# Kernel tuning notes

Measured on AMD Instinct MI355X. Metric: run time of the kernel, lower is better.

Reference implementation:

```python
import jax, jax.numpy as jnp
import numpy as np

KERNEL = 3            # MONAI default kernel_size
SMOOTH_NR = 0.0       # MONAI default
SMOOTH_DR = 1e-5      # MONAI default


def _box_sum_3d(x, k=KERNEL):
    """Separable 3D box-filter sum with zero padding ('same' output), over the
    three trailing spatial axes of a [B, C, X, Y, Z] tensor. Uses cumsum
    differences (one pass per axis) instead of 5 dense conv launches."""
    p = k // 2
    for ax in (2, 3, 4):
        pads = [(0, 0)] * x.ndim
        pads[ax] = (p + 1, p)  # extra leading zero so window sum = c[i+k]-c[i]
        c = jnp.cumsum(jnp.pad(x, pads), axis=ax)
        n = c.shape[ax]
        x = jax.lax.slice_in_dim(c, k, n, axis=ax) - jax.lax.slice_in_dim(c, 0, n - k, axis=ax)
    return x


def setup_inputs() -> dict:
    key = jax.random.key(0)
    k1, k2 = jax.random.split(key)
    shape = (2, 1, 192, 192, 192)
    pred = jax.random.uniform(k1, shape, dtype=jnp.float32)
    label = jax.random.uniform(k2, shape, dtype=jnp.float32)
    return {"pred": pred, "label": label}


def reference(pred, label):
    # Faithful to monai.losses.LocalNormalizedCrossCorrelationLoss defaults
    # (spatial_dims=3, rectangular kernel_size=3, reduction='mean').
    kernel_vol = jnp.asarray(float(KERNEL ** 3), dtype=pred.dtype)  # 27
    t, p = label, pred

    t_sum = _box_sum_3d(t)
    p_sum = _box_sum_3d(p)
    t2_sum = _box_sum_3d(t * t)
    p2_sum = _box_sum_3d(p * p)
    tp_sum = _box_sum_3d(t * p)

    t_avg = t_sum / kernel_vol
    p_avg = p_sum / kernel_vol

    cross = tp_sum - p_avg * t_sum                      # local cross-covariance * vol
    t_var = jnp.maximum(t2_sum - t_avg * t_sum, 0.0)    # local var * vol, clamped
    p_var = jnp.maximum(p2_sum - p_avg * p_sum, 0.0)

    ncc = (cross * cross + SMOOTH_NR) / (t_var * p_var + SMOOTH_DR)
    return -jnp.mean(ncc)
```

## Files before the change

### kernel.cpp

```cpp
#include <hip/hip_runtime.h>

typedef float v2f __attribute__((ext_vector_type(2)));

constexpr int NX = 192, NY = 192, NZ = 192, NB = 2;
constexpr int ZPT  = 4;
constexpr int TZ   = NZ / ZPT;
constexpr int BY   = 4;
constexpr int XSEG = 4;
constexpr int BLOCK_THREADS = TZ * BY;
constexpr int PLANE = NY * NZ;
constexpr int NXB = NX / XSEG;
constexpr int NYB = NY / BY;
constexpr int NBLK = NYB * NXB * NB;
constexpr int RSTR = 196;
constexpr int TILE_F = 2 * 6 * RSTR;

template<bool SAFE>
__device__ __forceinline__ void foldLDS(const float* __restrict__ buf,
    int ty, int z0, const float wy[3], int dm, int de, float wzm, float wze,
    float wx, v2f W[5][2])
{
    v2f S[5][3];
    #pragma unroll
    for (int r = 0; r < 3; ++r) {
        const float* Lt = buf + (ty + r) * RSTR;
        const float* Lp = Lt + 6 * RSTR;
        const float4 t4 = *reinterpret_cast<const float4*>(Lt + z0);
        const float4 p4 = *reinterpret_cast<const float4*>(Lp + z0);
        const float tm = Lt[z0 - dm] * wzm, te = Lt[z0 + de] * wze;
        const float pm = Lp[z0 - dm] * wzm, pe = Lp[z0 + de] * wze;
        v2f T[3]  = { v2f{tm, t4.x}, v2f{t4.y, t4.z}, v2f{t4.w, te} };
        v2f Pv[3] = { v2f{pm, p4.x}, v2f{p4.y, p4.z}, v2f{p4.w, pe} };
        if (!SAFE) {
            const float wr = wx * wy[r];
            #pragma unroll
            for (int q = 0; q < 3; ++q) { T[q] *= wr; Pv[q] *= wr; }
        }
        #pragma unroll
        for (int q = 0; q < 3; ++q) {
            if (r == 0) {
                S[0][q] = T[q];  S[1][q] = Pv[q];
                S[2][q] = T[q] * T[q];  S[3][q] = Pv[q] * Pv[q];  S[4][q] = T[q] * Pv[q];
            } else {
                S[0][q] += T[q];  S[1][q] += Pv[q];
                S[2][q] += T[q] * T[q];  S[3][q] += Pv[q] * Pv[q];  S[4][q] += T[q] * Pv[q];
            }
        }
    }
    #pragma unroll
    for (int q = 0; q < 5; ++q) {
        const float s0 = S[q][0].x, s1 = S[q][0].y, s2 = S[q][1].x;
        const float s3 = S[q][1].y, s4 = S[q][2].x, s5 = S[q][2].y;
        const float m12 = s1 + s2, m34 = s3 + s4;
        W[q][0] = v2f{s0 + m12, m12 + s3};
        W[q][1] = v2f{s2 + m34, m34 + s5};
    }
}

__device__ __forceinline__ float epilogue4(const v2f P[5][2], const v2f Wn[5][2])
{
    constexpr float inv_vol = 1.0f / 27.0f;
    float acc = 0.f;
    #pragma unroll
    for (int h = 0; h < 2; ++h) {
        const v2f st  = P[0][h] + Wn[0][h];
        const v2f sp  = P[1][h] + Wn[1][h];
        const v2f st2 = P[2][h] + Wn[2][h];
        const v2f sp2 = P[3][h] + Wn[3][h];
        const v2f stp = P[4][h] + Wn[4][h];
        const v2f tavg = st * inv_vol;
        const v2f pavg = sp * inv_vol;
        const v2f cross = stp - pavg * st;
        const v2f tvp   = st2 - tavg * st;
        const v2f pvp   = sp2 - pavg * sp;
        const v2f cc    = cross * cross;
        #pragma unroll
        for (int c = 0; c < 2; ++c) {
            const float tvar = fmaxf(tvp[c], 0.f);
            const float pvar = fmaxf(pvp[c], 0.f);
            acc += cc[c] * __builtin_amdgcn_rcpf(fmaf(tvar, pvar, 1e-5f));
        }
    }
    return acc;
}

template<bool SAFE>
__device__ __forceinline__ float march(
    const float* sb0, const float* sb1, const float* sb2,
    int lo0, int lo1, int lo2,
    float (*tile)[TILE_F],
    int ty, int z0, const float wy[3],
    int dm, int de, float wzm, float wze, int xs0)
{
    v2f U[5][2], V[5][2], P[5][2];
    float acc = 0.f;
    float4 G0, G1, G2;

#define XOFF(K) (SAFE ? (xs0 - 1 + (K)) * PLANE \
                      : min(max(xs0 - 1 + (K), 0), NX - 1) * PLANE)
#define WXK(K)  (SAFE ? 1.f : (((unsigned)(xs0 - 1 + (K)) < (unsigned)NX) ? 1.f : 0.f))
#define GLOAD(K) do { const int _xo = XOFF(K);                                  \
        G0 = *reinterpret_cast<const float4*>(sb0 + _xo);                       \
        G1 = *reinterpret_cast<const float4*>(sb1 + _xo);                       \
        G2 = *reinterpret_cast<const float4*>(sb2 + _xo); } while (0)
#define DSWR(K) do { float* _d = tile[(K) & 1];                                 \
        *reinterpret_cast<float4*>(_d + lo0) = G0;                              \
        *reinterpret_cast<float4*>(_d + lo1) = G1;                              \
        *reinterpret_cast<float4*>(_d + lo2) = G2; } while (0)
#define FOLD(K, WDST) foldLDS<SAFE>(tile[(K) & 1], ty, z0, wy, dm, de, wzm, wze, WXK(K), WDST)
#define PSET(A, B) do { _Pragma("unroll")                                       \
        for (int q = 0; q < 5; ++q) { _Pragma("unroll")                         \
            for (int h = 0; h < 2; ++h) P[q][h] = A[q][h] + B[q][h]; } } while (0)

    GLOAD(0); DSWR(0); __syncthreads();
    GLOAD(1); FOLD(0, U);             DSWR(1); __syncthreads();
    GLOAD(2); FOLD(1, V); PSET(U, V); DSWR(2); __syncthreads();
    GLOAD(3); FOLD(2, U); acc += epilogue4(P, U); PSET(V, U); DSWR(3); __syncthreads();
    GLOAD(4); FOLD(3, V); acc += epilogue4(P, V); PSET(U, V); DSWR(4); __syncthreads();
    GLOAD(5); FOLD(4, U); acc += epilogue4(P, U); PSET(V, U); DSWR(5); __syncthreads();
              FOLD(5, V); acc += epilogue4(P, V);

#undef XOFF
#undef WXK
#undef GLOAD
#undef DSWR
#undef FOLD
#undef PSET
    return acc;
}

__global__ __launch_bounds__(BLOCK_THREADS, 3)
void ncc_partial(const float* __restrict__ pred, const float* __restrict__ label,
                 float* __restrict__ partials)
{
    __shared__ alignas(16) float tile[2][TILE_F];

    const int tx  = threadIdx.x;
    const int ty  = threadIdx.y;
    const int tid = tx + ty * TZ;
    const int z0  = tx * ZPT;
    const int y0  = blockIdx.x * BY;
    const int y   = y0 + ty;
    const int xs0 = blockIdx.y * XSEG;
    const int b   = blockIdx.z;
    const int bbase = b * NX * PLANE;

    const float* sb[3];
    int lo[3];
    #pragma unroll
    for (int r = 0; r < 3; ++r) {
        const int j   = r * BLOCK_THREADS + tid;
        const int tt  = j / 288, rem = j - tt * 288;
        const int row = rem / 48, z4 = rem - row * 48;
        int grow = y0 - 1 + row;
        grow = min(max(grow, 0), NY - 1);
        sb[r] = (tt ? pred : label) + bbase + grow * NZ + z4 * 4;
        lo[r] = (tt * 6 + row) * RSTR + z4 * 4;
    }

    float wy[3];
    #pragma unroll
    for (int r = 0; r < 3; ++r) {
        const int yy = y + r - 1;
        wy[r] = ((unsigned)yy < (unsigned)NY) ? 1.f : 0.f;
    }
    const int   dm  = (tx == 0) ? 0 : 1;
    const int   de  = (tx == TZ - 1) ? 0 : ZPT;
    const float wzm = (tx == 0) ? 0.f : 1.f;
    const float wze = (tx == TZ - 1) ? 0.f : 1.f;

    const bool safe = (blockIdx.x >= 1) && (blockIdx.x <= NYB - 2) &&
                      (blockIdx.y >= 1) && (blockIdx.y <= NXB - 2);

    const float acc = safe
        ? march<true >(sb[0], sb[1], sb[2], lo[0], lo[1], lo[2], tile,
                       ty, z0, wy, dm, de, wzm, wze, xs0)
        : march<false>(sb[0], sb[1], sb[2], lo[0], lo[1], lo[2], tile,
                       ty, z0, wy, dm, de, wzm, wze, xs0);

    float a = acc;
    #pragma unroll
    for (int o = 32; o > 0; o >>= 1)
        a += __shfl_down(a, o, 64);

    __shared__ float wsum[BLOCK_THREADS / 64];
    if ((tid & 63) == 0) wsum[tid >> 6] = a;
    __syncthreads();
    if (tid == 0) {
        float s = 0.f;
        #pragma unroll
        for (int w = 0; w < BLOCK_THREADS / 64; ++w) s += wsum[w];
        partials[blockIdx.x + (int)gridDim.x * (blockIdx.y + (int)gridDim.y * blockIdx.z)] = s;
    }
}

__global__ __launch_bounds__(256)
void ncc_reduce(const float* __restrict__ partials, int n, float* __restrict__ out)
{
    __shared__ double sh[256];
    double s = 0.0;
    for (int i = threadIdx.x; i < n; i += 256) s += (double)partials[i];
    sh[threadIdx.x] = s;
    __syncthreads();
    for (int off = 128; off > 0; off >>= 1) {
        if ((int)threadIdx.x < off) sh[threadIdx.x] += sh[threadIdx.x + off];
        __syncthreads();
    }
    if (threadIdx.x == 0) {
        const double nvox = (double)NB * NX * NY * NZ;
        out[0] = (float)(-sh[0] / nvox);
    }
}

extern "C" void kernel_launch(void* const* d_in, const int* in_sizes, int n_in,
                              void* d_out, int out_size, void* d_ws, size_t ws_size,
                              hipStream_t stream) {
    const float* pred  = (const float*)d_in[0];
    const float* label = (const float*)d_in[1];
    float* out = (float*)d_out;
    float* partials = (float*)d_ws;

    dim3 block(TZ, BY, 1);
    dim3 grid(NYB, NXB, NB);

    ncc_partial<<<grid, block, 0, stream>>>(pred, label, partials);
    ncc_reduce<<<1, 256, 0, stream>>>(partials, NBLK, out);
}
```

Baseline: 49.60 us.

## Double x-segment per block and zero-pad LDS rows to drop z-edge masking

Each block now marches over 8 x-planes instead of 4, so the two halo planes loaded per segment are spread over more output planes and there are half as many blocks. The march is written as a rolled loop over two ping-pong LDS buffers. LDS rows gain zeroed pad cells at the z boundaries, which removes the per-thread z-edge offsets and weight multiplies in the fold. The cost is fewer blocks, which means less parallelism and a longer serial chain per block, and the halo layout becomes slightly more complex.

```diff
diff --git a/kernel.cpp b/kernel.cpp
--- a/kernel.cpp
+++ b/kernel.cpp
@@ -6,29 +6,30 @@
 constexpr int ZPT  = 4;
 constexpr int TZ   = NZ / ZPT;
 constexpr int BY   = 4;
-constexpr int XSEG = 4;
+constexpr int XSEG = 8;
 constexpr int BLOCK_THREADS = TZ * BY;
 constexpr int PLANE = NY * NZ;
 constexpr int NXB = NX / XSEG;
 constexpr int NYB = NY / BY;
 constexpr int NBLK = NYB * NXB * NB;
 constexpr int RSTR = 196;
-constexpr int TILE_F = 2 * 6 * RSTR;
+constexpr int NROWS = 12;
+constexpr int TILE_F = NROWS * RSTR + 4;
+constexpr int PADS   = (NROWS + 1) * 4;
 
 template<bool SAFE>
 __device__ __forceinline__ void foldLDS(const float* __restrict__ buf,
-    int ty, int z0, const float wy[3], int dm, int de, float wzm, float wze,
-    float wx, v2f W[5][2])
+    int ty, int z0, const float wy[3], float wx, v2f W[5][2])
 {
     v2f S[5][3];
     #pragma unroll
     for (int r = 0; r < 3; ++r) {
-        const float* Lt = buf + (ty + r) * RSTR;
+        const float* Lt = buf + 4 + (ty + r) * RSTR;
         const float* Lp = Lt + 6 * RSTR;
         const float4 t4 = *reinterpret_cast<const float4*>(Lt + z0);
         const float4 p4 = *reinterpret_cast<const float4*>(Lp + z0);
-        const float tm = Lt[z0 - dm] * wzm, te = Lt[z0 + de] * wze;
-        const float pm = Lp[z0 - dm] * wzm, pe = Lp[z0 + de] * wze;
+        const float tm = Lt[z0 - 1], te = Lt[z0 + 4];
+        const float pm = Lp[z0 - 1], pe = Lp[z0 + 4];
         v2f T[3]  = { v2f{tm, t4.x}, v2f{t4.y, t4.z}, v2f{t4.w, te} };
         v2f Pv[3] = { v2f{pm, p4.x}, v2f{p4.y, p4.z}, v2f{p4.w, pe} };
         if (!SAFE) {
@@ -87,10 +88,9 @@
 template<bool SAFE>
 __device__ __forceinline__ float march(
     const float* sb0, const float* sb1, const float* sb2,
-    int lo0, int lo1, int lo2,
+    int lo0, int lo1, int lo2, int padoff,
     float (*tile)[TILE_F],
-    int ty, int z0, const float wy[3],
-    int dm, int de, float wzm, float wze, int xs0)
+    int ty, int z0, const float wy[3], int xs0)
 {
     v2f U[5][2], V[5][2], P[5][2];
     float acc = 0.f;
@@ -103,22 +103,31 @@
         G0 = *reinterpret_cast<const float4*>(sb0 + _xo);                       \
         G1 = *reinterpret_cast<const float4*>(sb1 + _xo);                       \
         G2 = *reinterpret_cast<const float4*>(sb2 + _xo); } while (0)
-#define DSWR(K) do { float* _d = tile[(K) & 1];                                 \
+#define DSWR(B) do { float* _d = tile[(B)];                                     \
         *reinterpret_cast<float4*>(_d + lo0) = G0;                              \
         *reinterpret_cast<float4*>(_d + lo1) = G1;                              \
         *reinterpret_cast<float4*>(_d + lo2) = G2; } while (0)
-#define FOLD(K, WDST) foldLDS<SAFE>(tile[(K) & 1], ty, z0, wy, dm, de, wzm, wze, WXK(K), WDST)
+#define FOLD(B, K, WDST) foldLDS<SAFE>(tile[(B)], ty, z0, wy, WXK(K), WDST)
 #define PSET(A, B) do { _Pragma("unroll")                                       \
         for (int q = 0; q < 5; ++q) { _Pragma("unroll")                         \
             for (int h = 0; h < 2; ++h) P[q][h] = A[q][h] + B[q][h]; } } while (0)
 
-    GLOAD(0); DSWR(0); __syncthreads();
-    GLOAD(1); FOLD(0, U);             DSWR(1); __syncthreads();
-    GLOAD(2); FOLD(1, V); PSET(U, V); DSWR(2); __syncthreads();
-    GLOAD(3); FOLD(2, U); acc += epilogue4(P, U); PSET(V, U); DSWR(3); __syncthreads();
-    GLOAD(4); FOLD(3, V); acc += epilogue4(P, V); PSET(U, V); DSWR(4); __syncthreads();
-    GLOAD(5); FOLD(4, U); acc += epilogue4(P, U); PSET(V, U); DSWR(5); __syncthreads();
-              FOLD(5, V); acc += epilogue4(P, V);
+    GLOAD(0); DSWR(0);
+    if (padoff >= 0) { tile[0][padoff] = 0.f; tile[1][padoff] = 0.f; }
+    __syncthreads();
+    GLOAD(1); FOLD(0, 0, U);                DSWR(1); __syncthreads();
+    GLOAD(2); FOLD(1, 1, V); PSET(U, V);    DSWR(0); __syncthreads();
+
+    #pragma unroll 1
+    for (int k = 0; k < XSEG / 2 - 1; ++k) {
+        GLOAD(3 + 2 * k); FOLD(0, 2 + 2 * k, U);
+        acc += epilogue4(P, U); PSET(V, U); DSWR(1); __syncthreads();
+        GLOAD(4 + 2 * k); FOLD(1, 3 + 2 * k, V);
+        acc += epilogue4(P, V); PSET(U, V); DSWR(0); __syncthreads();
+    }
+
+    GLOAD(9); FOLD(0, 8, U); acc += epilogue4(P, U); PSET(V, U); DSWR(1); __syncthreads();
+              FOLD(1, 9, V); acc += epilogue4(P, V);
 
 #undef XOFF
 #undef WXK
@@ -155,8 +164,9 @@
         int grow = y0 - 1 + row;
         grow = min(max(grow, 0), NY - 1);
         sb[r] = (tt ? pred : label) + bbase + grow * NZ + z4 * 4;
-        lo[r] = (tt * 6 + row) * RSTR + z4 * 4;
-    }
+        lo[r] = (tt * 6 + row) * RSTR + 4 + z4 * 4;
+    }
+    const int padoff = (tid < PADS) ? (tid / 4) * RSTR + (tid & 3) : -1;
 
     float wy[3];
     #pragma unroll
@@ -164,19 +174,15 @@
         const int yy = y + r - 1;
         wy[r] = ((unsigned)yy < (unsigned)NY) ? 1.f : 0.f;
     }
-    const int   dm  = (tx == 0) ? 0 : 1;
-    const int   de  = (tx == TZ - 1) ? 0 : ZPT;
-    const float wzm = (tx == 0) ? 0.f : 1.f;
-    const float wze = (tx == TZ - 1) ? 0.f : 1.f;
 
     const bool safe = (blockIdx.x >= 1) && (blockIdx.x <= NYB - 2) &&
                       (blockIdx.y >= 1) && (blockIdx.y <= NXB - 2);
 
     const float acc = safe
-        ? march<true >(sb[0], sb[1], sb[2], lo[0], lo[1], lo[2], tile,
-                       ty, z0, wy, dm, de, wzm, wze, xs0)
-        : march<false>(sb[0], sb[1], sb[2], lo[0], lo[1], lo[2], tile,
-                       ty, z0, wy, dm, de, wzm, wze, xs0);
+        ? march<true >(sb[0], sb[1], sb[2], lo[0], lo[1], lo[2], padoff, tile,
+                       ty, z0, wy, xs0)
+        : march<false>(sb[0], sb[1], sb[2], lo[0], lo[1], lo[2], padoff, tile,
+                       ty, z0, wy, xs0);
 
     float a = acc;
     #pragma unroll
```

Result: slower. 55.00 us (+10.9%).

## Map each z-row to one wavefront and fetch z-halo via DPP shifts

Applied to the files above, without the earlier changes.

Changes the block shape to 64 z-threads of 3 voxels each, times 3 y-rows, so every z-row fills exactly one 64-lane wavefront. The z-neighbour halo values now come from wavefront shift-right/left DPP moves, whose bound control zeroes the edge lanes, instead of extra LDS reads with per-thread edge masks. The LDS tile drops its padded stride, and the cooperative global-to-LDS staging is redistributed with a predicated third load. The costs are a larger y-halo overhead (5 staged rows per 3 output rows), more blocks, and scalar stride-3 LDS reads in place of float4 reads.

```diff
diff --git a/kernel.cpp b/kernel.cpp
--- a/kernel.cpp
+++ b/kernel.cpp
@@ -3,71 +3,83 @@
 typedef float v2f __attribute__((ext_vector_type(2)));
 
 constexpr int NX = 192, NY = 192, NZ = 192, NB = 2;
-constexpr int ZPT  = 4;
+constexpr int ZPT  = 3;
 constexpr int TZ   = NZ / ZPT;
-constexpr int BY   = 4;
+constexpr int BY   = 3;
 constexpr int XSEG = 4;
 constexpr int BLOCK_THREADS = TZ * BY;
 constexpr int PLANE = NY * NZ;
+constexpr int NYT = NY / BY;
 constexpr int NXB = NX / XSEG;
-constexpr int NYB = NY / BY;
-constexpr int NBLK = NYB * NXB * NB;
-constexpr int RSTR = 196;
-constexpr int TILE_F = 2 * 6 * RSTR;
+constexpr int NBLK = NYT * NXB * NB;
+constexpr int ROWS = BY + 2;
+constexpr int TILE_F = 2 * ROWS * NZ;
+constexpr int SUNITS = 2 * ROWS * (NZ / 4);
+
+__device__ __forceinline__ float wshr1(float v) {
+    return __int_as_float(__builtin_amdgcn_update_dpp(
+        0, __float_as_int(v), 0x138, 0xf, 0xf, true));
+}
+__device__ __forceinline__ float wshl1(float v) {
+    return __int_as_float(__builtin_amdgcn_update_dpp(
+        0, __float_as_int(v), 0x130, 0xf, 0xf, true));
+}
 
 template<bool SAFE>
 __device__ __forceinline__ void foldLDS(const float* __restrict__ buf,
-    int ty, int z0, const float wy[3], int dm, int de, float wzm, float wze,
-    float wx, v2f W[5][2])
-{
-    v2f S[5][3];
+    int ty, int tx, const float wy[3], float wx, v2f W01[5], float W2[5])
+{
+    v2f S01[5], S23[5]; float S4[5];
     #pragma unroll
     for (int r = 0; r < 3; ++r) {
-        const float* Lt = buf + (ty + r) * RSTR;
-        const float* Lp = Lt + 6 * RSTR;
-        const float4 t4 = *reinterpret_cast<const float4*>(Lt + z0);
-        const float4 p4 = *reinterpret_cast<const float4*>(Lp + z0);
-        const float tm = Lt[z0 - dm] * wzm, te = Lt[z0 + de] * wze;
-        const float pm = Lp[z0 - dm] * wzm, pe = Lp[z0 + de] * wze;
-        v2f T[3]  = { v2f{tm, t4.x}, v2f{t4.y, t4.z}, v2f{t4.w, te} };
-        v2f Pv[3] = { v2f{pm, p4.x}, v2f{p4.y, p4.z}, v2f{p4.w, pe} };
+        const float* Lt = buf + (ty + r) * NZ + 3 * tx;
+        const float* Lp = Lt + ROWS * NZ;
+        float ta = Lt[0], tb = Lt[1], tc = Lt[2];
+        float pa = Lp[0], pb = Lp[1], pc = Lp[2];
+        float tm = wshr1(tc), te = wshl1(ta);
+        float pm = wshr1(pc), pe = wshl1(pa);
         if (!SAFE) {
             const float wr = wx * wy[r];
-            #pragma unroll
-            for (int q = 0; q < 3; ++q) { T[q] *= wr; Pv[q] *= wr; }
+            tm *= wr; ta *= wr; tb *= wr; tc *= wr; te *= wr;
+            pm *= wr; pa *= wr; pb *= wr; pc *= wr; pe *= wr;
         }
-        #pragma unroll
-        for (int q = 0; q < 3; ++q) {
-            if (r == 0) {
-                S[0][q] = T[q];  S[1][q] = Pv[q];
-                S[2][q] = T[q] * T[q];  S[3][q] = Pv[q] * Pv[q];  S[4][q] = T[q] * Pv[q];
-            } else {
-                S[0][q] += T[q];  S[1][q] += Pv[q];
-                S[2][q] += T[q] * T[q];  S[3][q] += Pv[q] * Pv[q];  S[4][q] += T[q] * Pv[q];
-            }
+        const v2f T01 = v2f{tm, ta}, T23 = v2f{tb, tc};
+        const v2f P01 = v2f{pm, pa}, P23 = v2f{pb, pc};
+        if (r == 0) {
+            S01[0] = T01;        S23[0] = T23;        S4[0] = te;
+            S01[1] = P01;        S23[1] = P23;        S4[1] = pe;
+            S01[2] = T01 * T01;  S23[2] = T23 * T23;  S4[2] = te * te;
+            S01[3] = P01 * P01;  S23[3] = P23 * P23;  S4[3] = pe * pe;
+            S01[4] = T01 * P01;  S23[4] = T23 * P23;  S4[4] = te * pe;
+        } else {
+            S01[0] += T01;        S23[0] += T23;        S4[0] += te;
+            S01[1] += P01;        S23[1] += P23;        S4[1] += pe;
+            S01[2] += T01 * T01;  S23[2] += T23 * T23;  S4[2] += te * te;
+            S01[3] += P01 * P01;  S23[3] += P23 * P23;  S4[3] += pe * pe;
+            S01[4] += T01 * P01;  S23[4] += T23 * P23;  S4[4] += te * pe;
         }
     }
     #pragma unroll
     for (int q = 0; q < 5; ++q) {
-        const float s0 = S[q][0].x, s1 = S[q][0].y, s2 = S[q][1].x;
-        const float s3 = S[q][1].y, s4 = S[q][2].x, s5 = S[q][2].y;
+        const float s0 = S01[q].x, s1 = S01[q].y, s2 = S23[q].x;
+        const float s3 = S23[q].y, s4 = S4[q];
         const float m12 = s1 + s2, m34 = s3 + s4;
-        W[q][0] = v2f{s0 + m12, m12 + s3};
-        W[q][1] = v2f{s2 + m34, m34 + s5};
-    }
-}
-
-__device__ __forceinline__ float epilogue4(const v2f P[5][2], const v2f Wn[5][2])
+        W01[q] = v2f{s0 + m12, m12 + s3};
+        W2[q]  = s2 + m34;
+    }
+}
+
+__device__ __forceinline__ float epilogue3(const v2f P01[5], const float P2[5],
+                                           const v2f W01[5], const float W2[5])
 {
     constexpr float inv_vol = 1.0f / 27.0f;
     float acc = 0.f;
-    #pragma unroll
-    for (int h = 0; h < 2; ++h) {
-        const v2f st  = P[0][h] + Wn[0][h];
-        const v2f sp  = P[1][h] + Wn[1][h];
-        const v2f st2 = P[2][h] + Wn[2][h];
-        const v2f sp2 = P[3][h] + Wn[3][h];
-        const v2f stp = P[4][h] + Wn[4][h];
+    {
+        const v2f st  = P01[0] + W01[0];
+        const v2f sp  = P01[1] + W01[1];
+        const v2f st2 = P01[2] + W01[2];
+        const v2f sp2 = P01[3] + W01[3];
+        const v2f stp = P01[4] + W01[4];
         const v2f tavg = st * inv_vol;
         const v2f pavg = sp * inv_vol;
         const v2f cross = stp - pavg * st;
@@ -81,18 +93,31 @@
             acc += cc[c] * __builtin_amdgcn_rcpf(fmaf(tvar, pvar, 1e-5f));
         }
     }
+    {
+        const float st  = P2[0] + W2[0];
+        const float sp  = P2[1] + W2[1];
+        const float st2 = P2[2] + W2[2];
+        const float sp2 = P2[3] + W2[3];
+        const float stp = P2[4] + W2[4];
+        const float tavg = st * inv_vol;
+        const float pavg = sp * inv_vol;
+        const float cross = fmaf(-pavg, st, stp);
+        const float tvar  = fmaxf(fmaf(-tavg, st, st2), 0.f);
+        const float pvar  = fmaxf(fmaf(-pavg, sp, sp2), 0.f);
+        acc += cross * cross * __builtin_amdgcn_rcpf(fmaf(tvar, pvar, 1e-5f));
+    }
     return acc;
 }
 
 template<bool SAFE>
 __device__ __forceinline__ float march(
-    const float* sb0, const float* sb1, const float* sb2,
+    const float* sb0, const float* sb1, const float* sb2, bool do3,
     int lo0, int lo1, int lo2,
     float (*tile)[TILE_F],
-    int ty, int z0, const float wy[3],
-    int dm, int de, float wzm, float wze, int xs0)
-{
-    v2f U[5][2], V[5][2], P[5][2];
+    int ty, int tx, const float wy[3], int xs0)
+{
+    v2f U01[5], V01[5], P01[5];
+    float U2[5], V2[5], P2[5];
     float acc = 0.f;
     float4 G0, G1, G2;
 
@@ -102,23 +127,26 @@
 #define GLOAD(K) do { const int _xo = XOFF(K);                                  \
         G0 = *reinterpret_cast<const float4*>(sb0 + _xo);                       \
         G1 = *reinterpret_cast<const float4*>(sb1 + _xo);                       \
-        G2 = *reinterpret_cast<const float4*>(sb2 + _xo); } while (0)
+        if (do3) G2 = *reinterpret_cast<const float4*>(sb2 + _xo); } while (0)
 #define DSWR(K) do { float* _d = tile[(K) & 1];                                 \
         *reinterpret_cast<float4*>(_d + lo0) = G0;                              \
         *reinterpret_cast<float4*>(_d + lo1) = G1;                              \
-        *reinterpret_cast<float4*>(_d + lo2) = G2; } while (0)
-#define FOLD(K, WDST) foldLDS<SAFE>(tile[(K) & 1], ty, z0, wy, dm, de, wzm, wze, WXK(K), WDST)
-#define PSET(A, B) do { _Pragma("unroll")                                       \
-        for (int q = 0; q < 5; ++q) { _Pragma("unroll")                         \
-            for (int h = 0; h < 2; ++h) P[q][h] = A[q][h] + B[q][h]; } } while (0)
+        if (do3) *reinterpret_cast<float4*>(_d + lo2) = G2; } while (0)
+#define FOLD(K, A01, A2) foldLDS<SAFE>(tile[(K) & 1], ty, tx, wy, WXK(K), A01, A2)
+#define PSET(A01, A2, B01, B2) do { _Pragma("unroll")                           \
+        for (int q = 0; q < 5; ++q) { P01[q] = A01[q] + B01[q];                 \
+                                      P2[q]  = A2[q]  + B2[q]; } } while (0)
 
     GLOAD(0); DSWR(0); __syncthreads();
-    GLOAD(1); FOLD(0, U);             DSWR(1); __syncthreads();
-    GLOAD(2); FOLD(1, V); PSET(U, V); DSWR(2); __syncthreads();
-    GLOAD(3); FOLD(2, U); acc += epilogue4(P, U); PSET(V, U); DSWR(3); __syncthreads();
-    GLOAD(4); FOLD(3, V); acc += epilogue4(P, V); PSET(U, V); DSWR(4); __syncthreads();
-    GLOAD(5); FOLD(4, U); acc += epilogue4(P, U); PSET(V, U); DSWR(5); __syncthreads();
-              FOLD(5, V); acc += epilogue4(P, V);
+    GLOAD(1); FOLD(0, U01, U2);                          DSWR(1); __syncthreads();
+    GLOAD(2); FOLD(1, V01, V2); PSET(U01, U2, V01, V2);  DSWR(2); __syncthreads();
+    GLOAD(3); FOLD(2, U01, U2); acc += epilogue3(P01, P2, U01, U2);
+              PSET(V01, V2, U01, U2);                    DSWR(3); __syncthreads();
+    GLOAD(4); FOLD(3, V01, V2); acc += epilogue3(P01, P2, V01, V2);
+              PSET(U01, U2, V01, V2);                    DSWR(4); __syncthreads();
+    GLOAD(5); FOLD(4, U01, U2); acc += epilogue3(P01, P2, U01, U2);
+              PSET(V01, V2, U01, U2);                    DSWR(5); __syncthreads();
+              FOLD(5, V01, V2); acc += epilogue3(P01, P2, V01, V2);
 
 #undef XOFF
 #undef WXK
@@ -138,25 +166,26 @@
     const int tx  = threadIdx.x;
     const int ty  = threadIdx.y;
     const int tid = tx + ty * TZ;
-    const int z0  = tx * ZPT;
-    const int y0  = blockIdx.x * BY;
-    const int y   = y0 + ty;
+    const int Y0  = blockIdx.x * BY;
+    const int y   = Y0 + ty;
     const int xs0 = blockIdx.y * XSEG;
     const int b   = blockIdx.z;
     const int bbase = b * NX * PLANE;
 
-    const float* sb[3];
-    int lo[3];
-    #pragma unroll
-    for (int r = 0; r < 3; ++r) {
-        const int j   = r * BLOCK_THREADS + tid;
-        const int tt  = j / 288, rem = j - tt * 288;
-        const int row = rem / 48, z4 = rem - row * 48;
-        int grow = y0 - 1 + row;
-        grow = min(max(grow, 0), NY - 1);
-        sb[r] = (tt ? pred : label) + bbase + grow * NZ + z4 * 4;
-        lo[r] = (tt * 6 + row) * RSTR + z4 * 4;
-    }
+    const float* sb[3]; int lo[3];
+    #pragma unroll
+    for (int k = 0; k < 3; ++k) {
+        const int u  = tid + k * BLOCK_THREADS;
+        const int uu = (u < SUNITS) ? u : 0;
+        const int tt  = uu / 240;
+        const int rem = uu - tt * 240;
+        const int row = rem / 48;
+        const int z4  = rem - row * 48;
+        const int grow = min(max(Y0 - 1 + row, 0), NY - 1);
+        sb[k] = (tt ? pred : label) + bbase + grow * NZ + z4 * 4;
+        lo[k] = (tt * ROWS + row) * NZ + z4 * 4;
+    }
+    const bool do3 = (tid < SUNITS - 2 * BLOCK_THREADS);
 
     float wy[3];
     #pragma unroll
@@ -164,19 +193,15 @@
         const int yy = y + r - 1;
         wy[r] = ((unsigned)yy < (unsigned)NY) ? 1.f : 0.f;
     }
-    const int   dm  = (tx == 0) ? 0 : 1;
-    const int   de  = (tx == TZ - 1) ? 0 : ZPT;
-    const float wzm = (tx == 0) ? 0.f : 1.f;
-    const float wze = (tx == TZ - 1) ? 0.f : 1.f;
-
-    const bool safe = (blockIdx.x >= 1) && (blockIdx.x <= NYB - 2) &&
+
+    const bool safe = (blockIdx.x >= 1) && (blockIdx.x <= NYT - 2) &&
                       (blockIdx.y >= 1) && (blockIdx.y <= NXB - 2);
 
     const float acc = safe
-        ? march<true >(sb[0], sb[1], sb[2], lo[0], lo[1], lo[2], tile,
-                       ty, z0, wy, dm, de, wzm, wze, xs0)
-        : march<false>(sb[0], sb[1], sb[2], lo[0], lo[1], lo[2], tile,
-                       ty, z0, wy, dm, de, wzm, wze, xs0);
+        ? march<true >(sb[0], sb[1], sb[2], do3, lo[0], lo[1], lo[2], tile,
+                       ty, tx, wy, xs0)
+        : march<false>(sb[0], sb[1], sb[2], do3, lo[0], lo[1], lo[2], tile,
+                       ty, tx, wy, xs0);
 
     float a = acc;
     #pragma unroll
@@ -221,7 +246,7 @@
     float* partials = (float*)d_ws;
 
     dim3 block(TZ, BY, 1);
-    dim3 grid(NYB, NXB, NB);
+    dim3 grid(NYT, NXB, NB);
 
     ncc_partial<<<grid, block, 0, stream>>>(pred, label, partials);
     ncc_reduce<<<1, 256, 0, stream>>>(partials, NBLK, out);
```

After: 147.2 us. 197% more time.

## Remap to one wavefront per z-row and swap z-halo LDS reads for DPP shifts

Applied to the files above, without the earlier changes.

Each thread now handles 3 z-values instead of 4, so one 64-lane wavefront covers a full 192-wide z row. The block grows to 6 y-rows, which cuts the y-halo overhead of the LDS tile from 6/4 to 8/6 rows and leaves one float4 global load per thread per tensor. The z-neighbour values are fetched with wave-shift DPP moves whose bound_ctrl gives zero padding, replacing the extra LDS loads and the edge-weight logic. The cost is a wasted fourth lane in the epilogue, now fed zeros, plus unaligned scalar LDS reads in place of float4 reads.

```diff
diff --git a/kernel.cpp b/kernel.cpp
--- a/kernel.cpp
+++ b/kernel.cpp
@@ -3,57 +3,68 @@
 typedef float v2f __attribute__((ext_vector_type(2)));
 
 constexpr int NX = 192, NY = 192, NZ = 192, NB = 2;
-constexpr int ZPT  = 4;
+constexpr int ZPT  = 3;
 constexpr int TZ   = NZ / ZPT;
-constexpr int BY   = 4;
+constexpr int BY   = 6;
 constexpr int XSEG = 4;
 constexpr int BLOCK_THREADS = TZ * BY;
 constexpr int PLANE = NY * NZ;
+constexpr int NYT = NY / BY;
 constexpr int NXB = NX / XSEG;
-constexpr int NYB = NY / BY;
-constexpr int NBLK = NYB * NXB * NB;
-constexpr int RSTR = 196;
-constexpr int TILE_F = 2 * 6 * RSTR;
+constexpr int NBLK = NYT * NXB * NB;
+constexpr int ROWS = BY + 2;
+constexpr int TILE_F = 2 * ROWS * NZ;
+
+__device__ __forceinline__ float wshr1(float v) {
+    return __int_as_float(__builtin_amdgcn_update_dpp(
+        0, __float_as_int(v), 0x138, 0xf, 0xf, true));
+}
+__device__ __forceinline__ float wshl1(float v) {
+    return __int_as_float(__builtin_amdgcn_update_dpp(
+        0, __float_as_int(v), 0x130, 0xf, 0xf, true));
+}
 
 template<bool SAFE>
 __device__ __forceinline__ void foldLDS(const float* __restrict__ buf,
-    int ty, int z0, const float wy[3], int dm, int de, float wzm, float wze,
-    float wx, v2f W[5][2])
-{
-    v2f S[5][3];
+    int ty, int tx, const float wy[3], float wx, v2f W[5][2])
+{
+    v2f SA[5], SB[5]; float SE[5];
     #pragma unroll
     for (int r = 0; r < 3; ++r) {
-        const float* Lt = buf + (ty + r) * RSTR;
-        const float* Lp = Lt + 6 * RSTR;
-        const float4 t4 = *reinterpret_cast<const float4*>(Lt + z0);
-        const float4 p4 = *reinterpret_cast<const float4*>(Lp + z0);
-        const float tm = Lt[z0 - dm] * wzm, te = Lt[z0 + de] * wze;
-        const float pm = Lp[z0 - dm] * wzm, pe = Lp[z0 + de] * wze;
-        v2f T[3]  = { v2f{tm, t4.x}, v2f{t4.y, t4.z}, v2f{t4.w, te} };
-        v2f Pv[3] = { v2f{pm, p4.x}, v2f{p4.y, p4.z}, v2f{p4.w, pe} };
+        const float* Lt = buf + (ty + r) * NZ + 3 * tx;
+        const float* Lp = Lt + ROWS * NZ;
+        float ta = Lt[0], tb = Lt[1], tc = Lt[2];
+        float pa = Lp[0], pb = Lp[1], pc = Lp[2];
+        float tm = wshr1(tc), te = wshl1(ta);
+        float pm = wshr1(pc), pe = wshl1(pa);
         if (!SAFE) {
             const float wr = wx * wy[r];
-            #pragma unroll
-            for (int q = 0; q < 3; ++q) { T[q] *= wr; Pv[q] *= wr; }
+            tm *= wr; ta *= wr; tb *= wr; tc *= wr; te *= wr;
+            pm *= wr; pa *= wr; pb *= wr; pc *= wr; pe *= wr;
         }
-        #pragma unroll
-        for (int q = 0; q < 3; ++q) {
-            if (r == 0) {
-                S[0][q] = T[q];  S[1][q] = Pv[q];
-                S[2][q] = T[q] * T[q];  S[3][q] = Pv[q] * Pv[q];  S[4][q] = T[q] * Pv[q];
-            } else {
-                S[0][q] += T[q];  S[1][q] += Pv[q];
-                S[2][q] += T[q] * T[q];  S[3][q] += Pv[q] * Pv[q];  S[4][q] += T[q] * Pv[q];
-            }
+        const v2f TA = v2f{tm, ta}, TB = v2f{tb, tc};
+        const v2f PA = v2f{pm, pa}, PB = v2f{pb, pc};
+        if (r == 0) {
+            SA[0] = TA;       SB[0] = TB;       SE[0] = te;
+            SA[1] = PA;       SB[1] = PB;       SE[1] = pe;
+            SA[2] = TA * TA;  SB[2] = TB * TB;  SE[2] = te * te;
+            SA[3] = PA * PA;  SB[3] = PB * PB;  SE[3] = pe * pe;
+            SA[4] = TA * PA;  SB[4] = TB * PB;  SE[4] = te * pe;
+        } else {
+            SA[0] += TA;       SB[0] += TB;       SE[0] += te;
+            SA[1] += PA;       SB[1] += PB;       SE[1] += pe;
+            SA[2] += TA * TA;  SB[2] += TB * TB;  SE[2] += te * te;
+            SA[3] += PA * PA;  SB[3] += PB * PB;  SE[3] += pe * pe;
+            SA[4] += TA * PA;  SB[4] += TB * PB;  SE[4] += te * pe;
         }
     }
     #pragma unroll
     for (int q = 0; q < 5; ++q) {
-        const float s0 = S[q][0].x, s1 = S[q][0].y, s2 = S[q][1].x;
-        const float s3 = S[q][1].y, s4 = S[q][2].x, s5 = S[q][2].y;
+        const float s0 = SA[q].x, s1 = SA[q].y, s2 = SB[q].x;
+        const float s3 = SB[q].y, s4 = SE[q];
         const float m12 = s1 + s2, m34 = s3 + s4;
         W[q][0] = v2f{s0 + m12, m12 + s3};
-        W[q][1] = v2f{s2 + m34, m34 + s5};
+        W[q][1] = v2f{s2 + m34, 0.f};
     }
 }
 
@@ -86,28 +97,25 @@
 
 template<bool SAFE>
 __device__ __forceinline__ float march(
-    const float* sb0, const float* sb1, const float* sb2,
-    int lo0, int lo1, int lo2,
+    const float* sb0, const float* sb1,
+    int lo0, int lo1,
     float (*tile)[TILE_F],
-    int ty, int z0, const float wy[3],
-    int dm, int de, float wzm, float wze, int xs0)
+    int ty, int tx, const float wy[3], int xs0)
 {
     v2f U[5][2], V[5][2], P[5][2];
     float acc = 0.f;
-    float4 G0, G1, G2;
+    float4 G0, G1;
 
 #define XOFF(K) (SAFE ? (xs0 - 1 + (K)) * PLANE \
                       : min(max(xs0 - 1 + (K), 0), NX - 1) * PLANE)
 #define WXK(K)  (SAFE ? 1.f : (((unsigned)(xs0 - 1 + (K)) < (unsigned)NX) ? 1.f : 0.f))
 #define GLOAD(K) do { const int _xo = XOFF(K);                                  \
         G0 = *reinterpret_cast<const float4*>(sb0 + _xo);                       \
-        G1 = *reinterpret_cast<const float4*>(sb1 + _xo);                       \
-        G2 = *reinterpret_cast<const float4*>(sb2 + _xo); } while (0)
+        G1 = *reinterpret_cast<const float4*>(sb1 + _xo); } while (0)
 #define DSWR(K) do { float* _d = tile[(K) & 1];                                 \
         *reinterpret_cast<float4*>(_d + lo0) = G0;                              \
-        *reinterpret_cast<float4*>(_d + lo1) = G1;                              \
-        *reinterpret_cast<float4*>(_d + lo2) = G2; } while (0)
-#define FOLD(K, WDST) foldLDS<SAFE>(tile[(K) & 1], ty, z0, wy, dm, de, wzm, wze, WXK(K), WDST)
+        *reinterpret_cast<float4*>(_d + lo1) = G1; } while (0)
+#define FOLD(K, WDST) foldLDS<SAFE>(tile[(K) & 1], ty, tx, wy, WXK(K), WDST)
 #define PSET(A, B) do { _Pragma("unroll")                                       \
         for (int q = 0; q < 5; ++q) { _Pragma("unroll")                         \
             for (int h = 0; h < 2; ++h) P[q][h] = A[q][h] + B[q][h]; } } while (0)
@@ -138,25 +146,19 @@
     const int tx  = threadIdx.x;
     const int ty  = threadIdx.y;
     const int tid = tx + ty * TZ;
-    const int z0  = tx * ZPT;
-    const int y0  = blockIdx.x * BY;
-    const int y   = y0 + ty;
+    const int Y0  = blockIdx.x * BY;
+    const int y   = Y0 + ty;
     const int xs0 = blockIdx.y * XSEG;
     const int b   = blockIdx.z;
     const int bbase = b * NX * PLANE;
 
-    const float* sb[3];
-    int lo[3];
-    #pragma unroll
-    for (int r = 0; r < 3; ++r) {
-        const int j   = r * BLOCK_THREADS + tid;
-        const int tt  = j / 288, rem = j - tt * 288;
-        const int row = rem / 48, z4 = rem - row * 48;
-        int grow = y0 - 1 + row;
-        grow = min(max(grow, 0), NY - 1);
-        sb[r] = (tt ? pred : label) + bbase + grow * NZ + z4 * 4;
-        lo[r] = (tt * 6 + row) * RSTR + z4 * 4;
-    }
+    const int row = tid / 48;
+    const int z4  = tid - row * 48;
+    const int grow = min(max(Y0 - 1 + row, 0), NY - 1);
+    const float* sb0 = label + bbase + grow * NZ + z4 * 4;
+    const float* sb1 = pred  + bbase + grow * NZ + z4 * 4;
+    const int lo0 = row * NZ + z4 * 4;
+    const int lo1 = lo0 + ROWS * NZ;
 
     float wy[3];
     #pragma unroll
@@ -164,19 +166,13 @@
         const int yy = y + r - 1;
         wy[r] = ((unsigned)yy < (unsigned)NY) ? 1.f : 0.f;
     }
-    const int   dm  = (tx == 0) ? 0 : 1;
-    const int   de  = (tx == TZ - 1) ? 0 : ZPT;
-    const float wzm = (tx == 0) ? 0.f : 1.f;
-    const float wze = (tx == TZ - 1) ? 0.f : 1.f;
-
-    const bool safe = (blockIdx.x >= 1) && (blockIdx.x <= NYB - 2) &&
+
+    const bool safe = (blockIdx.x >= 1) && (blockIdx.x <= NYT - 2) &&
                       (blockIdx.y >= 1) && (blockIdx.y <= NXB - 2);
 
     const float acc = safe
-        ? march<true >(sb[0], sb[1], sb[2], lo[0], lo[1], lo[2], tile,
-                       ty, z0, wy, dm, de, wzm, wze, xs0)
-        : march<false>(sb[0], sb[1], sb[2], lo[0], lo[1], lo[2], tile,
-                       ty, z0, wy, dm, de, wzm, wze, xs0);
+        ? march<true >(sb0, sb1, lo0, lo1, tile, ty, tx, wy, xs0)
+        : march<false>(sb0, sb1, lo0, lo1, tile, ty, tx, wy, xs0);
 
     float a = acc;
     #pragma unroll
@@ -221,7 +217,7 @@
     float* partials = (float*)d_ws;
 
     dim3 block(TZ, BY, 1);
-    dim3 grid(NYB, NXB, NB);
+    dim3 grid(NYT, NXB, NB);
 
     ncc_partial<<<grid, block, 0, stream>>>(pred, label, partials);
     ncc_reduce<<<1, 256, 0, stream>>>(partials, NBLK, out);
```

Measured after the change: 72.37 us. 45.9% more time.
